# Kernel tuning notes

Hardware: AMD Instinct MI355X
Metric: run time of the kernel (lower is better)

## Reference

```python
import jax, jax.numpy as jnp
import numpy as np

N_FFT = 64
HOP = 32
PAD = N_FFT // 2

def _window():
    # torch.hann_window(n_fft) is periodic: 0.5*(1 - cos(2*pi*n/N))
    n = jnp.arange(N_FFT, dtype=jnp.float32)
    return 0.5 * (1.0 - jnp.cos(2.0 * jnp.pi * n / N_FFT))

def _frame_idx(n_frames):
    return jnp.arange(n_frames)[:, None] * HOP + jnp.arange(N_FFT)[None, :]

def _stft(x):
    # x: [..., T] -> complex spectrogram [..., n_frames, F] (torch center=True, reflect pad)
    xp = jnp.pad(x, [(0, 0)] * (x.ndim - 1) + [(PAD, PAD)], mode='reflect')
    Tp = xp.shape[-1]
    n_frames = (Tp - N_FFT) // HOP + 1
    frames = xp[..., _frame_idx(n_frames)] * _window()  # [..., n_frames, n_fft]
    return jnp.fft.rfft(frames, axis=-1)

def _istft(spec, T):
    # spec: [..., n_frames, F] -> signal [..., T] (torch istft with length=T)
    w = _window()
    frames = jnp.fft.irfft(spec, n=N_FFT, axis=-1) * w  # [..., n_frames, n_fft]
    n_frames = frames.shape[-2]
    Tp = T + 2 * PAD
    idx = _frame_idx(n_frames)
    ola = jnp.zeros(frames.shape[:-2] + (Tp,), frames.dtype).at[..., idx].add(frames)
    env = jnp.zeros((Tp,), frames.dtype).at[idx].add(w * w)
    env = jnp.where(env > 1e-11, env, 1.0)
    return (ola / env)[..., PAD:PAD + T]

def reference(x, weight):
    # x: [B, C_in, T], weight: [C_out, C_in, F]
    B, C, T = x.shape
    U = _stft(x)  # [B, C_in, n_frames, F] complex
    # Linearity: sum over input channels in frequency domain, then one ISTFT per output channel.
    Yr = jnp.einsum('oif,binf->bonf', weight, U.real)
    Yi = jnp.einsum('oif,binf->bonf', weight, U.imag)
    Y = Yr + 1j * Yi  # [B, C_out, n_frames, F]
    return _istft(Y, T)  # [B, C_out, T]

def setup_inputs() -> dict:
    key = jax.random.key(0)
    k1, k2 = jax.random.split(key)
    B, C_in, C_out, T = 8, 64, 64, 16384
    x = jax.random.normal(k1, (B, C_in, T), dtype=jnp.float32)
    weight = jax.random.normal(k2, (C_out, C_in, N_FFT // 2 + 1), dtype=jnp.float32)
    return {"x": x, "weight": weight}
```

## Files before the change

### kernel.cpp

```cpp
#include <hip/hip_runtime.h>
#include <cstddef>

#define TT 16384
#define NFRAMES 513
#define NFP 520
#define BNP (8 * NFP)
#define PI32 0.09817477042468103870f

typedef unsigned int u32;
typedef unsigned short u16;
typedef __attribute__((ext_vector_type(8))) short bf16x8;
typedef __attribute__((ext_vector_type(4))) float f32x4;

#define TAB_WBF 0
#define TAB_BM  (33 * 64 * 72)
#define TAB_BTA (TAB_BM + 80 * 72)
#define TAB_TOT (TAB_BTA + 64 * 72)
#define TF_EINV 0

__device__ __forceinline__ float b2f(u16 h) {
  union { u32 u; float f; } v; v.u = ((u32)h) << 16; return v.f;
}
__device__ __forceinline__ u16 f2b(float f) {
  union { float f; u32 u; } v; v.f = f;
  const u32 r = v.u + 0x7FFFu + ((v.u >> 16) & 1u);
  return (u16)(r >> 16);
}
__device__ __forceinline__ u32 pack2(float a, float b) {
  return (u32)f2b(a) | ((u32)f2b(b) << 16);
}

__global__ __launch_bounds__(256) void k0_tables(const float* __restrict__ W,
                                                 u16* __restrict__ t16,
                                                 float* __restrict__ tf) {
  const int b = blockIdx.x, tid = threadIdx.x;
  if (b < 33) {
    for (int idx = tid; idx < 64 * 72; idx += 256) {
      const int o = idx / 72, i = idx % 72;
      const float v = (i < 64) ? W[(size_t)(o * 64 + i) * 33 + b] : 0.f;
      t16[TAB_WBF + b * 64 * 72 + idx] = f2b(v);
    }
  } else if (b == 33) {
    for (int idx = tid; idx < 80 * 72; idx += 256) {
      const int fc = idx / 72, j = idx % 72;
      float v = 0.f;
      if (j < 64 && fc < 65) {
        const float wj = 0.5f * (1.0f - cosf((float)j * PI32));
        if (fc < 64) {
          const int f = fc >> 1;
          const float ang = (float)((f * j) & 63) * PI32;
          v = wj * ((fc & 1) ? -sinf(ang) : cosf(ang));
        } else {
          v = (j & 1) ? -wj : wj;
        }
      }
      t16[TAB_BM + idx] = f2b(v);
    }
  } else {
    for (int idx = tid; idx < 64 * 72; idx += 256) {
      const int j = idx / 72, cf = idx % 72;
      float v = 0.f;
      if (cf < 65) {
        const int f = cf >> 1;
        const float wj = 0.5f * (1.0f - cosf((float)j * PI32));
        const float sc = ((f == 0) || (f == 32)) ? 0.015625f : 0.03125f;
        const float ang = (float)((f * j) & 63) * PI32;
        v = wj * sc * ((cf & 1) ? -sinf(ang) : cosf(ang));
      }
      t16[TAB_BTA + idx] = f2b(v);
    }
    if (tid < 32) {
      const float c = cosf((float)tid * PI32);
      tf[TF_EINV + tid] = 2.0f / (1.0f + c * c);
    }
  }
}

__global__ __launch_bounds__(256) void k1_stft(const float* __restrict__ x,
                                               const u16* __restrict__ t16,
                                               u16* __restrict__ U) {
  const int tile = blockIdx.x;
  const int ch   = blockIdx.y;
  const int b    = blockIdx.z;
  const int tid = threadIdx.x;
  __shared__ __align__(16) u16 Bm[80 * 72];
  __shared__ __align__(16) u16 Awt[64 * 72];
  __shared__ __align__(16) u16 Cs[66 * 72];
  __shared__ float xef[64];

  for (int k = tid; k < 720; k += 256)
    ((uint4*)Bm)[k] = ((const uint4*)(t16 + TAB_BM))[k];

  const float* xb = x + (size_t)(b * 64 + ch) * TT;

  if (tile == 8) {
    if (tid < 64) {
      const int t = (tid < 32) ? (16352 + tid) : (16414 - tid);
      xef[tid] = xb[t];
    }
    __syncthreads();
    if (tid < 66) {
      float s = 0.f;
#pragma unroll 8
      for (int j = 0; j < 64; ++j)
        s = fmaf(xef[j], b2f(Bm[tid * 72 + j]), s);
      U[(size_t)(tid * 64 + ch) * BNP + b * NFP + 512] = f2b(s);
    }
    return;
  }

  const int F0 = tile * 64;
  if (tile == 0) {
    if (tid < 32) Awt[tid] = f2b(xb[32 - tid]);
    for (int c = 8 + tid; c < 520; c += 256) {
      const float4 v = *(const float4*)(xb + 4 * c - 32);
      const uint2 pk = make_uint2(pack2(v.x, v.y), pack2(v.z, v.w));
      const int flb = c >> 3, jj = 4 * (c & 7);
      if (flb < 64) *(uint2*)&Awt[flb * 72 + jj] = pk;
      *(uint2*)&Awt[(flb - 1) * 72 + 32 + jj] = pk;
    }
  } else {
    const float* src = xb + 32 * F0 - 32;
    for (int c = tid; c < 520; c += 256) {
      const float4 v = *(const float4*)(src + 4 * c);
      const uint2 pk = make_uint2(pack2(v.x, v.y), pack2(v.z, v.w));
      const int flb = c >> 3, jj = 4 * (c & 7);
      if (flb < 64) *(uint2*)&Awt[flb * 72 + jj] = pk;
      if (flb >= 1) *(uint2*)&Awt[(flb - 1) * 72 + 32 + jj] = pk;
    }
  }
  __syncthreads();

  const int wave = tid >> 6, lane = tid & 63;
  const int n = lane & 15, quad = lane >> 4;

  bf16x8 bfr[4][2];
#pragma unroll
  for (int nt = 0; nt < 4; ++nt)
#pragma unroll
    for (int ks = 0; ks < 2; ++ks)
      bfr[nt][ks] = *(const bf16x8*)&Awt[(nt * 16 + n) * 72 + ks * 32 + quad * 8];

  const int npass = (wave == 0) ? 2 : 1;
  for (int pass = 0; pass < npass; ++pass) {
    const int mt = pass ? 4 : wave;
    bf16x8 af[2];
#pragma unroll
    for (int ks = 0; ks < 2; ++ks)
      af[ks] = *(const bf16x8*)&Bm[(mt * 16 + n) * 72 + ks * 32 + quad * 8];
    f32x4 acc[4];
#pragma unroll
    for (int nt = 0; nt < 4; ++nt) acc[nt] = (f32x4){0.f, 0.f, 0.f, 0.f};
#pragma unroll
    for (int ks = 0; ks < 2; ++ks)
#pragma unroll
      for (int nt = 0; nt < 4; ++nt)
        acc[nt] = __builtin_amdgcn_mfma_f32_16x16x32_bf16(af[ks], bfr[nt][ks],
                                                          acc[nt], 0, 0, 0);
#pragma unroll
    for (int nt = 0; nt < 4; ++nt) {
      const int fl = nt * 16 + n;
#pragma unroll
      for (int r = 0; r < 4; ++r) {
        const int fc = mt * 16 + quad * 4 + r;
        if (fc < 66) Cs[fc * 72 + fl] = f2b(acc[nt][r]);
      }
    }
  }
  __syncthreads();

  const int bnb = b * NFP + F0;
  for (int k = tid; k < 528; k += 256) {
    const int fc = k >> 3, part = k & 7;
    *(uint4*)(U + (size_t)(fc * 64 + ch) * BNP + bnb + part * 8) =
        *(const uint4*)&Cs[fc * 72 + part * 8];
  }
}

__global__ __launch_bounds__(256) void k2_mix(const u16* __restrict__ t16,
                                              u16* __restrict__ U) {
  const int f   = blockIdx.y;
  const int bn0 = blockIdx.x * 64;
  const int tid = threadIdx.x;
  __shared__ __align__(16) u16 Ut[2 * 64 * 72];
  __shared__ __align__(16) u16 Wl[64 * 72];

  for (int k = tid; k < 576; k += 256)
    ((uint4*)Wl)[k] = ((const uint4*)(t16 + TAB_WBF + f * 64 * 72))[k];

#pragma unroll
  for (int kk = 0; kk < 4; ++kk) {
    const int id = tid + kk * 256;
    const int c = id >> 9, rem = id & 511;
    const int i = rem >> 3, qc = rem & 7;
    const uint4 raw = *(const uint4*)(U + (size_t)((2 * f + c) * 64 + i) * BNP + bn0 + 8 * qc);
    const int col = (((i >> 3) ^ qc) << 3) + (i & 7);
    u16* base = &Ut[c * 4608 + col];
#pragma unroll
    for (int e = 0; e < 8; ++e) {
      const u32 w = ((const u32*)&raw)[e >> 1];
      base[(8 * qc + e) * 72] = (u16)((e & 1) ? (w >> 16) : (w & 0xFFFFu));
    }
  }
  __syncthreads();

  const int wave = tid >> 6, lane = tid & 63;
  const int n = lane & 15, quad = lane >> 4;
  const int mt = wave;

  bf16x8 af[2];
#pragma unroll
  for (int ks = 0; ks < 2; ++ks)
    af[ks] = *(const bf16x8*)&Wl[(mt * 16 + n) * 72 + ks * 32 + quad * 8];

  f32x4 acc[4][2];
#pragma unroll
  for (int nt = 0; nt < 4; ++nt)
#pragma unroll
    for (int c = 0; c < 2; ++c) acc[nt][c] = (f32x4){0.f, 0.f, 0.f, 0.f};

#pragma unroll
  for (int ks = 0; ks < 2; ++ks)
#pragma unroll
    for (int nt = 0; nt < 4; ++nt) {
      const int q = nt * 16 + n;
      const int chunk = (((ks << 2) + quad) ^ ((q >> 3) & 7)) << 3;
#pragma unroll
      for (int c = 0; c < 2; ++c) {
        const bf16x8 bf = *(const bf16x8*)&Ut[c * 4608 + q * 72 + chunk];
        acc[nt][c] = __builtin_amdgcn_mfma_f32_16x16x32_bf16(af[ks], bf,
                                                             acc[nt][c], 0, 0, 0);
      }
    }
  __syncthreads();

#pragma unroll
  for (int nt = 0; nt < 4; ++nt) {
    const int col = nt * 16 + n;
#pragma unroll
    for (int c = 0; c < 2; ++c)
#pragma unroll
      for (int r = 0; r < 4; ++r) {
        const int o = mt * 16 + quad * 4 + r;
        Ut[(c * 64 + o) * 72 + col] = f2b(acc[nt][c][r]);
      }
  }
  __syncthreads();

  for (int k = tid; k < 1024; k += 256) {
    const int row = k >> 3, part = k & 7;
    const int c = row >> 6, o = row & 63;
    *(uint4*)(U + (size_t)((2 * f + c) * 64 + o) * BNP + bn0 + part * 8) =
        *(const uint4*)&Ut[row * 72 + part * 8];
  }
}

__global__ __launch_bounds__(256, 6) void k3_istft(const u16* __restrict__ Y,
                                                   const u16* __restrict__ t16,
                                                   const float* __restrict__ tf,
                                                   float* __restrict__ out) {
  const int tile = blockIdx.x;
  const int o    = blockIdx.y;
  const int b    = blockIdx.z;
  const int n0 = tile * 64;
  const int tid = threadIdx.x;
  __shared__ __align__(16) u16 BtA[64 * 72];
  __shared__ __align__(16) u16 Yt[80 * 64];
  __shared__ __align__(16) u16 y64[72];
  __shared__ __align__(16) float einv[32];

  for (int k = tid; k < 576; k += 256)
    ((uint4*)BtA)[k] = ((const uint4*)(t16 + TAB_BTA))[k];

  const size_t ybase = (size_t)b * NFP + n0;
  for (int id = tid; id < 576; id += 256) {
    const int cf = id / 9, oct = id % 9;
    const uint4 raw = *(const uint4*)(Y + (size_t)(cf * 64 + o) * BNP + ybase + oct * 8);
    const u16* s = (const u16*)&raw;
#pragma unroll
    for (int e = 0; e < 8; ++e) {
      const int row = oct * 8 + e;
      const int sw = (row ^ (row >> 3)) & 7;
      Yt[row * 64 + ((((cf >> 3) ^ sw) << 3) | (cf & 7))] = s[e];
    }
  }
  if (tid < 9)
    *(uint4*)&y64[tid * 8] =
        *(const uint4*)(Y + (size_t)(64 * 64 + o) * BNP + ybase + tid * 8);
  if (tid < 32) einv[tid] = tf[TF_EINV + tid];
  __syncthreads();

  const int wave = tid >> 6, lane = tid & 63;
  const int n = lane & 15, quad = lane >> 4;

  const int jrowA = wave * 8 + (n & 7) + (n >> 3) * 32;
  bf16x8 af[2];
#pragma unroll
  for (int ks = 0; ks < 2; ++ks)
    af[ks] = *(const bf16x8*)&BtA[jrowA * 72 + ks * 32 + quad * 8];

  float a64v[4];
#pragma unroll
  for (int r = 0; r < 4; ++r) {
    const int c = quad * 4 + r;
    const int j = wave * 8 + (c & 7) + (c >> 3) * 32;
    a64v[r] = b2f(BtA[j * 72 + 64]);
  }

  f32x4 acc[5];
#pragma unroll
  for (int nt = 0; nt < 5; ++nt) acc[nt] = (f32x4){0.f, 0.f, 0.f, 0.f};
#pragma unroll
  for (int nt = 0; nt < 5; ++nt) {
    const int row = nt * 16 + n;
    const int sw = (row ^ (row >> 3)) & 7;
    const u16* yrow = &Yt[row * 64];
#pragma unroll
    for (int ks = 0; ks < 2; ++ks) {
      const bf16x8 bf = *(const bf16x8*)&yrow[((ks * 4 + quad) ^ sw) << 3];
      acc[nt] = __builtin_amdgcn_mfma_f32_16x16x32_bf16(af[ks], bf, acc[nt], 0, 0, 0);
    }
  }

  const int srcl = (((n + 15) & 15) | ((2 | (quad & 1)) << 4)) << 2;
  const float4 ev = *(const float4*)&einv[wave * 8 + (quad & 1) * 4];
  float* pob = out + (size_t)(b * 64 + o) * TT + 32 * n0 + wave * 8 + (quad & 1) * 4;
  float hiPrev[4] = {0.f, 0.f, 0.f, 0.f};
#pragma unroll
  for (int nt = 0; nt < 5; ++nt) {
    const int fl = nt * 16 + n;
    if (nt < 4 || n == 0) {
      const float yv = b2f(y64[fl]);
#pragma unroll
      for (int r = 0; r < 4; ++r) acc[nt][r] = fmaf(yv, a64v[r], acc[nt][r]);
    }
    float cur[4];
#pragma unroll
    for (int r = 0; r < 4; ++r)
      cur[r] = __int_as_float(
          __builtin_amdgcn_ds_bpermute(srcl, __float_as_int(acc[nt][r])));
    if (quad < 2) {
      const bool valid = (nt < 4) ? (fl > 0) : (n == 0);
      if (valid) {
        float v[4];
#pragma unroll
        for (int r = 0; r < 4; ++r)
          v[r] = (acc[nt][r] + ((n == 0) ? hiPrev[r] : cur[r])) * ev[r];
        *(float4*)(pob + (fl - 1) * 32) = make_float4(v[0], v[1], v[2], v[3]);
      }
    }
#pragma unroll
    for (int r = 0; r < 4; ++r) hiPrev[r] = cur[r];
  }
}

extern "C" void kernel_launch(void* const* d_in, const int* in_sizes, int n_in,
                              void* d_out, int out_size, void* d_ws, size_t ws_size,
                              hipStream_t stream) {
  const float* x  = (const float*)d_in[0];
  const float* wt = (const float*)d_in[1];
  float* out = (float*)d_out;
  u16* U = (u16*)d_ws;
  u16* t16 = (u16*)((char*)d_ws + (size_t)66 * 64 * BNP * 2);
  float* tf = (float*)(t16 + TAB_TOT);

  dim3 blk(256);
  k0_tables<<<dim3(35),       blk, 0, stream>>>(wt, t16, tf);
  k1_stft  <<<dim3(9, 64, 8), blk, 0, stream>>>(x, t16, U);
  k2_mix   <<<dim3(65, 33),   blk, 0, stream>>>(t16, U);
  k3_istft <<<dim3(8, 64, 8), blk, 0, stream>>>(U, t16, tf, out);
}
```

Measured before the change: 139.8 us.

## Process two batches per STFT block with prefetched input and double-buffered tile

```diff
diff --git a/kernel.cpp b/kernel.cpp
--- a/kernel.cpp
+++ b/kernel.cpp
@@ -81,100 +81,149 @@
                                                u16* __restrict__ U) {
   const int tile = blockIdx.x;
   const int ch   = blockIdx.y;
-  const int b    = blockIdx.z;
+  const int bz   = blockIdx.z;
   const int tid = threadIdx.x;
   __shared__ __align__(16) u16 Bm[80 * 72];
-  __shared__ __align__(16) u16 Awt[64 * 72];
+  __shared__ __align__(16) u16 Awt[2][64 * 72];
   __shared__ __align__(16) u16 Cs[66 * 72];
-  __shared__ float xef[64];
+  __shared__ float xef[2][64];
 
   for (int k = tid; k < 720; k += 256)
     ((uint4*)Bm)[k] = ((const uint4*)(t16 + TAB_BM))[k];
 
-  const float* xb = x + (size_t)(b * 64 + ch) * TT;
-
   if (tile == 8) {
-    if (tid < 64) {
-      const int t = (tid < 32) ? (16352 + tid) : (16414 - tid);
-      xef[tid] = xb[t];
+    if (tid < 128) {
+      const int c = tid >> 6, j = tid & 63;
+      const int t = (j < 32) ? (16352 + j) : (16414 - j);
+      xef[c][j] = x[(size_t)((bz + 4 * c) * 64 + ch) * TT + t];
     }
     __syncthreads();
-    if (tid < 66) {
+    for (int id = tid; id < 132; id += 256) {
+      const int c = id / 66, fc = id % 66;
       float s = 0.f;
 #pragma unroll 8
       for (int j = 0; j < 64; ++j)
-        s = fmaf(xef[j], b2f(Bm[tid * 72 + j]), s);
-      U[(size_t)(tid * 64 + ch) * BNP + b * NFP + 512] = f2b(s);
+        s = fmaf(xef[c][j], b2f(Bm[fc * 72 + j]), s);
+      U[(size_t)(fc * 64 + ch) * BNP + (bz + 4 * c) * NFP + 512] = f2b(s);
     }
     return;
   }
 
   const int F0 = tile * 64;
-  if (tile == 0) {
-    if (tid < 32) Awt[tid] = f2b(xb[32 - tid]);
-    for (int c = 8 + tid; c < 520; c += 256) {
-      const float4 v = *(const float4*)(xb + 4 * c - 32);
-      const uint2 pk = make_uint2(pack2(v.x, v.y), pack2(v.z, v.w));
-      const int flb = c >> 3, jj = 4 * (c & 7);
-      if (flb < 64) *(uint2*)&Awt[flb * 72 + jj] = pk;
-      *(uint2*)&Awt[(flb - 1) * 72 + 32 + jj] = pk;
-    }
-  } else {
-    const float* src = xb + 32 * F0 - 32;
-    for (int c = tid; c < 520; c += 256) {
-      const float4 v = *(const float4*)(src + 4 * c);
-      const uint2 pk = make_uint2(pack2(v.x, v.y), pack2(v.z, v.w));
-      const int flb = c >> 3, jj = 4 * (c & 7);
-      if (flb < 64) *(uint2*)&Awt[flb * 72 + jj] = pk;
-      if (flb >= 1) *(uint2*)&Awt[(flb - 1) * 72 + 32 + jj] = pk;
-    }
-  }
-  __syncthreads();
-
   const int wave = tid >> 6, lane = tid & 63;
   const int n = lane & 15, quad = lane >> 4;
 
+  auto issue = [&](const float* xb, float4* v, float& rf) {
+    if (tile == 0) {
+      if (tid < 32) rf = xb[32 - tid];
+      v[0] = *(const float4*)(xb + 4 * (8 + tid) - 32);
+      v[1] = *(const float4*)(xb + 4 * (264 + tid) - 32);
+    } else {
+      const float* src = xb + 32 * F0 - 32;
+      v[0] = *(const float4*)(src + 4 * tid);
+      v[1] = *(const float4*)(src + 4 * (tid + 256));
+      if (tid < 8) v[2] = *(const float4*)(src + 4 * (tid + 512));
+    }
+  };
+  auto writeA = [&](u16* Aw, const float4* v, float rf) {
+    if (tile == 0) {
+      if (tid < 32) Aw[tid] = f2b(rf);
+#pragma unroll
+      for (int q = 0; q < 2; ++q) {
+        const int c = 8 + tid + 256 * q;
+        const uint2 pk = make_uint2(pack2(v[q].x, v[q].y), pack2(v[q].z, v[q].w));
+        const int flb = c >> 3, jj = 4 * (c & 7);
+        if (flb < 64) *(uint2*)&Aw[flb * 72 + jj] = pk;
+        *(uint2*)&Aw[(flb - 1) * 72 + 32 + jj] = pk;
+      }
+    } else {
+#pragma unroll
+      for (int q = 0; q < 3; ++q) {
+        if (q == 2 && tid >= 8) continue;
+        const int c = tid + 256 * q;
+        const uint2 pk = make_uint2(pack2(v[q].x, v[q].y), pack2(v[q].z, v[q].w));
+        const int flb = c >> 3, jj = 4 * (c & 7);
+        if (flb < 64) *(uint2*)&Aw[flb * 72 + jj] = pk;
+        if (flb >= 1) *(uint2*)&Aw[(flb - 1) * 72 + 32 + jj] = pk;
+      }
+    }
+  };
+
+  bf16x8 afm[2], afx[2];
+
   bf16x8 bfr[4][2];
-#pragma unroll
-  for (int nt = 0; nt < 4; ++nt)
+  auto frag = [&](const u16* Aw) {
+#pragma unroll
+    for (int nt = 0; nt < 4; ++nt)
+#pragma unroll
+      for (int ks = 0; ks < 2; ++ks)
+        bfr[nt][ks] = *(const bf16x8*)&Aw[(nt * 16 + n) * 72 + ks * 32 + quad * 8];
+  };
+  auto computeCs = [&]() {
+    const int npass = (wave == 0) ? 2 : 1;
+    for (int pass = 0; pass < npass; ++pass) {
+      const bf16x8* af = pass ? afx : afm;
+      const int mt = pass ? 4 : wave;
+      f32x4 acc[4];
+#pragma unroll
+      for (int nt = 0; nt < 4; ++nt) acc[nt] = (f32x4){0.f, 0.f, 0.f, 0.f};
+#pragma unroll
+      for (int ks = 0; ks < 2; ++ks)
+#pragma unroll
+        for (int nt = 0; nt < 4; ++nt)
+          acc[nt] = __builtin_amdgcn_mfma_f32_16x16x32_bf16(af[ks], bfr[nt][ks],
+                                                            acc[nt], 0, 0, 0);
+#pragma unroll
+      for (int nt = 0; nt < 4; ++nt) {
+        const int fl = nt * 16 + n;
+#pragma unroll
+        for (int r = 0; r < 4; ++r) {
+          const int fc = mt * 16 + quad * 4 + r;
+          if (fc < 66) Cs[fc * 72 + fl] = f2b(acc[nt][r]);
+        }
+      }
+    }
+  };
+  auto copyout = [&](int beff) {
+    const int bnb = beff * NFP + F0;
+    for (int k = tid; k < 528; k += 256) {
+      const int fc = k >> 3, part = k & 7;
+      *(uint4*)(U + (size_t)(fc * 64 + ch) * BNP + bnb + part * 8) =
+          *(const uint4*)&Cs[fc * 72 + part * 8];
+    }
+  };
+
+  const float* xbA = x + (size_t)(bz * 64 + ch) * TT;
+  const float* xbB = x + (size_t)((bz + 4) * 64 + ch) * TT;
+
+  float4 va[3] = {}; float ra = 0.f;
+  issue(xbA, va, ra);
+  writeA(Awt[0], va, ra);
+  __syncthreads();
+
+#pragma unroll
+  for (int ks = 0; ks < 2; ++ks)
+    afm[ks] = *(const bf16x8*)&Bm[(wave * 16 + n) * 72 + ks * 32 + quad * 8];
+  if (wave == 0) {
 #pragma unroll
     for (int ks = 0; ks < 2; ++ks)
-      bfr[nt][ks] = *(const bf16x8*)&Awt[(nt * 16 + n) * 72 + ks * 32 + quad * 8];
-
-  const int npass = (wave == 0) ? 2 : 1;
-  for (int pass = 0; pass < npass; ++pass) {
-    const int mt = pass ? 4 : wave;
-    bf16x8 af[2];
-#pragma unroll
-    for (int ks = 0; ks < 2; ++ks)
-      af[ks] = *(const bf16x8*)&Bm[(mt * 16 + n) * 72 + ks * 32 + quad * 8];
-    f32x4 acc[4];
-#pragma unroll
-    for (int nt = 0; nt < 4; ++nt) acc[nt] = (f32x4){0.f, 0.f, 0.f, 0.f};
-#pragma unroll
-    for (int ks = 0; ks < 2; ++ks)
-#pragma unroll
-      for (int nt = 0; nt < 4; ++nt)
-        acc[nt] = __builtin_amdgcn_mfma_f32_16x16x32_bf16(af[ks], bfr[nt][ks],
-                                                          acc[nt], 0, 0, 0);
-#pragma unroll
-    for (int nt = 0; nt < 4; ++nt) {
-      const int fl = nt * 16 + n;
-#pragma unroll
-      for (int r = 0; r < 4; ++r) {
-        const int fc = mt * 16 + quad * 4 + r;
-        if (fc < 66) Cs[fc * 72 + fl] = f2b(acc[nt][r]);
-      }
-    }
-  }
-  __syncthreads();
-
-  const int bnb = b * NFP + F0;
-  for (int k = tid; k < 528; k += 256) {
-    const int fc = k >> 3, part = k & 7;
-    *(uint4*)(U + (size_t)(fc * 64 + ch) * BNP + bnb + part * 8) =
-        *(const uint4*)&Cs[fc * 72 + part * 8];
-  }
+      afx[ks] = *(const bf16x8*)&Bm[(64 + n) * 72 + ks * 32 + quad * 8];
+  }
+
+  frag(Awt[0]);
+  float4 vb[3] = {}; float rb = 0.f;
+  issue(xbB, vb, rb);
+  computeCs();
+  __syncthreads();
+
+  copyout(bz);
+  writeA(Awt[1], vb, rb);
+  __syncthreads();
+
+  frag(Awt[1]);
+  computeCs();
+  __syncthreads();
+  copyout(bz + 4);
 }
 
 __global__ __launch_bounds__(256) void k2_mix(const u16* __restrict__ t16,
@@ -366,7 +415,7 @@
 
   dim3 blk(256);
   k0_tables<<<dim3(35),       blk, 0, stream>>>(wt, t16, tf);
-  k1_stft  <<<dim3(9, 64, 8), blk, 0, stream>>>(x, t16, U);
+  k1_stft  <<<dim3(9, 64, 4), blk, 0, stream>>>(x, t16, U);
   k2_mix   <<<dim3(65, 33),   blk, 0, stream>>>(t16, U);
   k3_istft <<<dim3(8, 64, 8), blk, 0, stream>>>(U, t16, tf, out);
 }
```

Result: faster. 135.0 us (-3.4%).
